# Optimization experiments

Hardware: AMD Instinct MI355X
Metric: run time of the kernel (lower is better)

## Reference

```python
import jax, jax.numpy as jnp
import numpy as np

B, C, H, W_ = 128, 2048, 14, 14
N_DESC, N_ANS = 32, 1845


def setup_inputs() -> dict:
    key = jax.random.key(0)
    k1, k2, k3, k4, k5 = jax.random.split(key, 5)
    mask = jax.random.uniform(k1, (B, 1, H, W_), dtype=jnp.float32)
    features = jax.random.normal(k2, (B, C, H, W_), dtype=jnp.float32)
    instance = jax.random.randint(k3, (B,), 0, N_DESC, dtype=jnp.int64)
    Wt = jax.random.normal(k4, (N_DESC, N_ANS, C), dtype=jnp.float32) * 0.02
    b = jax.random.normal(k5, (N_DESC, N_ANS), dtype=jnp.float32) * 0.02
    return {"mask": mask, "features": features, "instance": instance, "W": Wt, "b": b}


def reference(mask, features, instance, W, b):
    Bsz, Cc, Hh, Ww = features.shape
    feat_flat = features.reshape(Bsz, Cc, Hh * Ww)            # [B,C,HW]
    mask_flat = mask.reshape(Bsz, 1, Hh * Ww)                 # [B,1,HW]
    attended = jnp.mean(mask_flat * feat_flat, axis=2)        # [B,C]
    Wi = W[instance]                                          # [B,A,C] per-sample weight gather
    bi = b[instance]                                          # [B,A]
    preds = jnp.einsum('bc,bac->ba', attended, Wi) + bi       # grouped small GEMM
    return preds
```

## Files before the change

kernel.cpp:

```cpp
#include <hip/hip_runtime.h>

#define BSZ   128
#define CC    2048
#define HW    196
#define NDESC 32
#define NANS  1845
#define ATILES ((NANS + 7) / 8)

typedef float f4 __attribute__((ext_vector_type(4)));

__global__ __launch_bounds__(256) void attend_group_kernel(
        const float* __restrict__ mask,
        const float* __restrict__ feat,
        const int*  __restrict__ inst,
        float* __restrict__ attended,
        int* __restrict__ counts,
        int* __restrict__ lists) {
    int row  = blockIdx.x * 4 + (threadIdx.x >> 6);
    int lane = threadIdx.x & 63;
    int b    = row >> 11;

    const f4* frow = (const f4*)(feat + (size_t)row * HW);
    const f4* mrow = (const f4*)(mask + (size_t)b * HW);

    float partial = 0.f;
    if (lane < 49) {
        f4 f = frow[lane];
        f4 m = mrow[lane];
        partial = f.x * m.x + f.y * m.y + f.z * m.z + f.w * m.w;
    }
    #pragma unroll
    for (int off = 32; off; off >>= 1)
        partial += __shfl_xor(partial, off, 64);
    if (lane == 0) attended[row] = partial * (1.f / 196.f);

    if (blockIdx.x == 0) {
        int t = threadIdx.x;
        if (t < NDESC) counts[t] = 0;
        __syncthreads();
        if (t < BSZ) {
            int i = inst[t];
            int slot = atomicAdd(&counts[i], 1);
            lists[i * BSZ + slot] = t;
        }
    }
}

__global__ __launch_bounds__(256) void gemm_kernel(
        const float* __restrict__ attended,
        const float* __restrict__ W,
        const float* __restrict__ bias,
        const int* __restrict__ counts,
        const int* __restrict__ lists,
        float* __restrict__ out) {
    int ins  = blockIdx.x / ATILES;
    int tile = blockIdx.x % ATILES;
    int cnt  = counts[ins];
    if (cnt == 0) return;

    int wid  = threadIdx.x >> 6;
    int lane = threadIdx.x & 63;
    int a0   = tile * 8 + wid * 2;
    int a1   = a0 + 1;
    bool v0  = a0 < NANS;
    bool v1  = a1 < NANS;

    const float* Wb = W + (size_t)ins * NANS * CC;

    f4 w0[8], w1[8];
    if (v0) {
        const f4* wr = (const f4*)(Wb + (size_t)a0 * CC) + lane;
        #pragma unroll
        for (int k = 0; k < 8; ++k) w0[k] = __builtin_nontemporal_load(wr + k * 64);
    }
    if (v1) {
        const f4* wr = (const f4*)(Wb + (size_t)a1 * CC) + lane;
        #pragma unroll
        for (int k = 0; k < 8; ++k) w1[k] = __builtin_nontemporal_load(wr + k * 64);
    }
    float b0 = v0 ? bias[ins * NANS + a0] : 0.f;
    float b1 = v1 ? bias[ins * NANS + a1] : 0.f;

    const int* lst = lists + ins * BSZ;

    for (int j = 0; j < cnt; j += 2) {
        int  bj0 = lst[j];
        bool h1  = (j + 1) < cnt;
        int  bj1 = h1 ? lst[j + 1] : bj0;
        const f4* ar0 = (const f4*)(attended + (size_t)bj0 * CC) + lane;
        const f4* ar1 = (const f4*)(attended + (size_t)bj1 * CC) + lane;

        float acc00 = 0.f, acc01 = 0.f, acc10 = 0.f, acc11 = 0.f;
        #pragma unroll
        for (int k = 0; k < 8; ++k) {
            f4 x = ar0[k * 64];
            f4 y = ar1[k * 64];
            acc00 += x.x * w0[k].x + x.y * w0[k].y + x.z * w0[k].z + x.w * w0[k].w;
            acc01 += x.x * w1[k].x + x.y * w1[k].y + x.z * w1[k].z + x.w * w1[k].w;
            acc10 += y.x * w0[k].x + y.y * w0[k].y + y.z * w0[k].z + y.w * w0[k].w;
            acc11 += y.x * w1[k].x + y.y * w1[k].y + y.z * w1[k].z + y.w * w1[k].w;
        }
        #pragma unroll
        for (int off = 32; off; off >>= 1) {
            acc00 += __shfl_xor(acc00, off, 64);
            acc01 += __shfl_xor(acc01, off, 64);
            acc10 += __shfl_xor(acc10, off, 64);
            acc11 += __shfl_xor(acc11, off, 64);
        }
        if (lane == 0) {
            if (v0) out[(size_t)bj0 * NANS + a0] = acc00 + b0;
            if (v1) out[(size_t)bj0 * NANS + a1] = acc01 + b1;
            if (h1) {
                if (v0) out[(size_t)bj1 * NANS + a0] = acc10 + b0;
                if (v1) out[(size_t)bj1 * NANS + a1] = acc11 + b1;
            }
        }
    }
}

extern "C" void kernel_launch(void* const* d_in, const int* in_sizes, int n_in,
                              void* d_out, int out_size, void* d_ws, size_t ws_size,
                              hipStream_t stream) {
    const float* mask = (const float*)d_in[0];
    const float* feat = (const float*)d_in[1];
    const int*   inst = (const int*)d_in[2];
    const float* W    = (const float*)d_in[3];
    const float* bias = (const float*)d_in[4];
    float*       out  = (float*)d_out;

    float* attended = (float*)d_ws;
    int*   counts   = (int*)((char*)d_ws + (size_t)BSZ * CC * sizeof(float));
    int*   lists    = counts + NDESC;

    attend_group_kernel<<<(BSZ * CC) / 4, 256, 0, stream>>>(
        mask, feat, inst, attended, counts, lists);
    gemm_kernel<<<NDESC * ATILES, 256, 0, stream>>>(
        attended, W, bias, counts, lists, out);
}
```

Before: 745.1 us.

## Stage attended rows in double-buffered LDS and enlarge GEMM tiles with XCD swizzle

```diff
diff --git a/kernel.cpp b/kernel.cpp
--- a/kernel.cpp
+++ b/kernel.cpp
@@ -5,7 +5,10 @@
 #define HW    196
 #define NDESC 32
 #define NANS  1845
-#define ATILES ((NANS + 7) / 8)
+
+#define TROWS  16
+#define ATILES ((NANS + TROWS - 1) / TROWS)
+#define GRID2  (NDESC * ATILES)
 
 typedef float f4 __attribute__((ext_vector_type(4)));
 
@@ -46,21 +49,24 @@
     }
 }
 
-__global__ __launch_bounds__(256) void gemm_kernel(
+__global__ __launch_bounds__(512) void gemm_kernel(
         const float* __restrict__ attended,
         const float* __restrict__ W,
         const float* __restrict__ bias,
         const int* __restrict__ counts,
         const int* __restrict__ lists,
         float* __restrict__ out) {
-    int ins  = blockIdx.x / ATILES;
-    int tile = blockIdx.x % ATILES;
-    int cnt  = counts[ins];
+    int bid     = blockIdx.x;
+    int logical = (bid & 7) * (GRID2 / 8) + (bid >> 3);
+    int ins     = logical / ATILES;
+    int tile    = logical % ATILES;
+    int cnt     = counts[ins];
     if (cnt == 0) return;
 
-    int wid  = threadIdx.x >> 6;
-    int lane = threadIdx.x & 63;
-    int a0   = tile * 8 + wid * 2;
+    int tid  = threadIdx.x;
+    int wid  = tid >> 6;
+    int lane = tid & 63;
+    int a0   = tile * TROWS + wid * 2;
     int a1   = a0 + 1;
     bool v0  = a0 < NANS;
     bool v1  = a1 < NANS;
@@ -81,39 +87,34 @@
     float b0 = v0 ? bias[ins * NANS + a0] : 0.f;
     float b1 = v1 ? bias[ins * NANS + a1] : 0.f;
 
+    __shared__ float lds[2][CC];
     const int* lst = lists + ins * BSZ;
 
-    for (int j = 0; j < cnt; j += 2) {
-        int  bj0 = lst[j];
-        bool h1  = (j + 1) < cnt;
-        int  bj1 = h1 ? lst[j + 1] : bj0;
-        const f4* ar0 = (const f4*)(attended + (size_t)bj0 * CC) + lane;
-        const f4* ar1 = (const f4*)(attended + (size_t)bj1 * CC) + lane;
+    f4 stage = *((const f4*)(attended + (size_t)lst[0] * CC) + tid);
 
-        float acc00 = 0.f, acc01 = 0.f, acc10 = 0.f, acc11 = 0.f;
+    for (int j = 0; j < cnt; ++j) {
+        int buf = j & 1;
+        ((f4*)lds[buf])[tid] = stage;
+        if (j + 1 < cnt)
+            stage = *((const f4*)(attended + (size_t)lst[j + 1] * CC) + tid);
+        __syncthreads();
+
+        float acc0 = 0.f, acc1 = 0.f;
         #pragma unroll
         for (int k = 0; k < 8; ++k) {
-            f4 x = ar0[k * 64];
-            f4 y = ar1[k * 64];
-            acc00 += x.x * w0[k].x + x.y * w0[k].y + x.z * w0[k].z + x.w * w0[k].w;
-            acc01 += x.x * w1[k].x + x.y * w1[k].y + x.z * w1[k].z + x.w * w1[k].w;
-            acc10 += y.x * w0[k].x + y.y * w0[k].y + y.z * w0[k].z + y.w * w0[k].w;
-            acc11 += y.x * w1[k].x + y.y * w1[k].y + y.z * w1[k].z + y.w * w1[k].w;
+            f4 x = ((const f4*)lds[buf])[lane + k * 64];
+            acc0 += x.x * w0[k].x + x.y * w0[k].y + x.z * w0[k].z + x.w * w0[k].w;
+            acc1 += x.x * w1[k].x + x.y * w1[k].y + x.z * w1[k].z + x.w * w1[k].w;
         }
         #pragma unroll
         for (int off = 32; off; off >>= 1) {
-            acc00 += __shfl_xor(acc00, off, 64);
-            acc01 += __shfl_xor(acc01, off, 64);
-            acc10 += __shfl_xor(acc10, off, 64);
-            acc11 += __shfl_xor(acc11, off, 64);
+            acc0 += __shfl_xor(acc0, off, 64);
+            acc1 += __shfl_xor(acc1, off, 64);
         }
         if (lane == 0) {
-            if (v0) out[(size_t)bj0 * NANS + a0] = acc00 + b0;
-            if (v1) out[(size_t)bj0 * NANS + a1] = acc01 + b1;
-            if (h1) {
-                if (v0) out[(size_t)bj1 * NANS + a0] = acc10 + b0;
-                if (v1) out[(size_t)bj1 * NANS + a1] = acc11 + b1;
-            }
+            int bj = lst[j];
+            if (v0) out[(size_t)bj * NANS + a0] = acc0 + b0;
+            if (v1) out[(size_t)bj * NANS + a1] = acc1 + b1;
         }
     }
 }
@@ -134,6 +135,6 @@
 
     attend_group_kernel<<<(BSZ * CC) / 4, 256, 0, stream>>>(
         mask, feat, inst, attended, counts, lists);
-    gemm_kernel<<<NDESC * ATILES, 256, 0, stream>>>(
+    gemm_kernel<<<GRID2, 512, 0, stream>>>(
         attended, W, bias, counts, lists, out);
 }
```

After: 717.6 us. -3.7%, faster.
